# Kernel optimization log

Measured on AMD Instinct MI355X. Metric: run time of the kernel, lower is better.

## Reference

```python
import jax, jax.numpy as jnp
import numpy as np

P = 2          # inverse-distance power (init arg p)
EPS = 1e-6     # clamp floor on dis**p
B, N, D, VDIM = 4096, 8192, 512, 512


def setup_inputs() -> dict:
    key = jax.random.key(0)
    kb, kk, kv = jax.random.split(key, 3)
    b = jax.random.normal(kb, (B, D), dtype=jnp.float32)
    K = jax.random.normal(kk, (N, D), dtype=jnp.float32)   # stacked sample keys
    V = jax.random.normal(kv, (N, VDIM), dtype=jnp.float32)  # stacked sample values
    return {"b": b, "K": K, "V": V}


def reference(b, K, V):
    # Pairwise Euclidean distances via the expansion ||b-k||^2 = ||b||^2 + ||k||^2 - 2 b.k
    # (avoids materializing the [B, N, D] difference tensor).
    b_sq = jnp.sum(b * b, axis=1, keepdims=True)          # [B, 1]
    k_sq = jnp.sum(K * K, axis=1)[None, :]                # [1, N]
    d2 = b_sq + k_sq - 2.0 * (b @ K.T)                    # [B, N]
    dist = jnp.sqrt(jnp.maximum(d2, 0.0))                 # torch.norm(k - b, dim=1)
    w = 1.0 / jnp.maximum(dist ** P, EPS)                 # 1 / clamp(dis^p, 1e-6)
    sum_w = jnp.sum(w, axis=1, keepdims=True)             # [B, 1]
    sum_v = w @ V                                         # sum_n w[b,n] * V[n,:]
    return sum_v / sum_w
```

## Files before the change

kernel.cpp:

```cpp
#include <hip/hip_runtime.h>
#include <stdint.h>

typedef __attribute__((ext_vector_type(2))) float  f32x2;
typedef __attribute__((ext_vector_type(4))) float  f32x4;
typedef __attribute__((ext_vector_type(2))) __bf16 bf16x2;
typedef __attribute__((ext_vector_type(8))) __bf16 bf16x8;

#define N_B    4096
#define N_K    8192
#define DDIM   512
#define VD     512
#define SPLITK 4

#define GLL(g, l) __builtin_amdgcn_global_load_lds(                      \
    (const __attribute__((address_space(1))) void*)(g),                  \
    (__attribute__((address_space(3))) void*)(l), 16, 0, 0)

__global__ void prep_rows(const float* __restrict__ src, __bf16* __restrict__ dst,
                          float* __restrict__ sq)
{
  const int row = blockIdx.x;
  const int tid = threadIdx.x;
  f32x2 v = ((const f32x2*)(src + (size_t)row * DDIM))[tid];
  float ss = v[0] * v[0] + v[1] * v[1];
  bf16x2 o; o[0] = (__bf16)v[0]; o[1] = (__bf16)v[1];
  ((bf16x2*)(dst + (size_t)row * DDIM))[tid] = o;
  #pragma unroll
  for (int m = 1; m < 64; m <<= 1) ss += __shfl_xor(ss, m);
  __shared__ float red[4];
  if ((tid & 63) == 0) red[tid >> 6] = ss;
  __syncthreads();
  if (tid == 0) sq[row] = red[0] + red[1] + red[2] + red[3];
}

__global__ void prep_vT(const float* __restrict__ V, __bf16* __restrict__ VT)
{
  __shared__ __bf16 t[64][72];
  const int n0 = blockIdx.x * 64;
  const int d0 = blockIdx.y * 64;
  const int tid = threadIdx.x;
  const int lr = tid >> 4, lc = tid & 15;
  #pragma unroll
  for (int p = 0; p < 4; p++) {
    const int r = p * 16 + lr;
    f32x4 v = *(const f32x4*)(V + (size_t)(n0 + r) * VD + d0 + lc * 4);
    t[r][lc * 4 + 0] = (__bf16)v[0];
    t[r][lc * 4 + 1] = (__bf16)v[1];
    t[r][lc * 4 + 2] = (__bf16)v[2];
    t[r][lc * 4 + 3] = (__bf16)v[3];
  }
  __syncthreads();
  const int od = tid >> 6, oc = tid & 63;
  #pragma unroll
  for (int p = 0; p < 16; p++) {
    const int d = p * 4 + od;
    VT[(size_t)(d0 + d) * N_K + n0 + oc] = t[oc][d];
  }
}

template<int MODE>
__global__ void __launch_bounds__(256, 2)
gemm_bt(const __bf16* __restrict__ Amat, const __bf16* __restrict__ Bmat,
        const int ldaE, const int ldbE, const int kPerSplit,
        const float* __restrict__ bsq, const float* __restrict__ ksq,
        __bf16* __restrict__ Wout, float* __restrict__ sumw,
        float* __restrict__ Pout)
{
  __shared__ __bf16 Asm[128 * 64];
  __shared__ __bf16 Bsm[128 * 64];

  const int tid  = threadIdx.x;
  const int wid  = tid >> 6;
  const int lane = tid & 63;
  const int wm = wid >> 1, wn = wid & 1;
  const int r15 = lane & 15, hi = lane >> 4;

  const int m0 = blockIdx.y * 128;
  const int n0 = blockIdx.x * 128;
  const long kBegin = (long)blockIdx.z * kPerSplit;

  const int srow   = lane >> 3;
  const int schunk = (lane & 7) ^ srow;

  const __bf16* aSrc = Amat + (size_t)(m0 + wid * 32 + srow) * ldaE + kBegin + schunk * 8;
  const __bf16* bSrc = Bmat + (size_t)(n0 + wid * 32 + srow) * ldbE + kBegin + schunk * 8;
  __bf16* aDst = &Asm[wid * 32 * 64];
  __bf16* bDst = &Bsm[wid * 32 * 64];

  const f32x4 fzero = {0.f, 0.f, 0.f, 0.f};
  f32x4 acc[4][4];
  #pragma unroll
  for (int i = 0; i < 4; i++)
    #pragma unroll
    for (int j = 0; j < 4; j++) acc[i][j] = fzero;

  for (int k0 = 0; k0 < kPerSplit; k0 += 64) {
    __syncthreads();
    #pragma unroll
    for (int i = 0; i < 4; i++) {
      GLL(aSrc + (size_t)i * 8 * ldaE + k0, aDst + i * 8 * 64);
      GLL(bSrc + (size_t)i * 8 * ldbE + k0, bDst + i * 8 * 64);
    }
    __syncthreads();
    #pragma unroll
    for (int kk = 0; kk < 2; kk++) {
      bf16x8 af[4], bfr[4];
      #pragma unroll
      for (int mf = 0; mf < 4; mf++) {
        const int cs = ((kk << 2) + hi) ^ (r15 & 7);
        af[mf] = *(const bf16x8*)((const char*)Asm +
                   (wm * 64 + mf * 16 + r15) * 128 + cs * 16);
      }
      #pragma unroll
      for (int nf = 0; nf < 4; nf++) {
        const int cs = ((kk << 2) + hi) ^ (r15 & 7);
        bfr[nf] = *(const bf16x8*)((const char*)Bsm +
                    (wn * 64 + nf * 16 + r15) * 128 + cs * 16);
      }
      #pragma unroll
      for (int mf = 0; mf < 4; mf++)
        #pragma unroll
        for (int nf = 0; nf < 4; nf++)
          acc[mf][nf] = __builtin_amdgcn_mfma_f32_16x16x32_bf16(
              af[mf], bfr[nf], acc[mf][nf], 0, 0, 0);
    }
  }

  if constexpr (MODE == 0) {
    float kq[4];
    #pragma unroll
    for (int nf = 0; nf < 4; nf++) kq[nf] = ksq[n0 + wn * 64 + nf * 16 + r15];
    #pragma unroll
    for (int mf = 0; mf < 4; mf++) {
      const int rowb = m0 + wm * 64 + mf * 16 + hi * 4;
      const f32x4 bq = *(const f32x4*)(bsq + rowb);
      float rsum[4] = {0.f, 0.f, 0.f, 0.f};
      #pragma unroll
      for (int nf = 0; nf < 4; nf++) {
        const int col = n0 + wn * 64 + nf * 16 + r15;
        #pragma unroll
        for (int r = 0; r < 4; r++) {
          const float d2 = bq[r] + kq[nf] - 2.0f * acc[mf][nf][r];
          const float w  = 1.0f / fmaxf(d2, 1e-6f);
          rsum[r] += w;
          Wout[(size_t)(rowb + r) * N_K + col] = (__bf16)w;
        }
      }
      #pragma unroll
      for (int r = 0; r < 4; r++) {
        float tsum = rsum[r];
        tsum += __shfl_xor(tsum, 1);
        tsum += __shfl_xor(tsum, 2);
        tsum += __shfl_xor(tsum, 4);
        tsum += __shfl_xor(tsum, 8);
        if (r15 == 0) atomicAdd(&sumw[rowb + r], tsum);
      }
    }
  } else {
    float* op = Pout + (size_t)blockIdx.z * N_B * VD;
    #pragma unroll
    for (int mf = 0; mf < 4; mf++) {
      const int rowb = m0 + wm * 64 + mf * 16 + hi * 4;
      #pragma unroll
      for (int nf = 0; nf < 4; nf++) {
        const int col = n0 + wn * 64 + nf * 16 + r15;
        #pragma unroll
        for (int r = 0; r < 4; r++)
          op[(size_t)(rowb + r) * VD + col] = acc[mf][nf][r];
      }
    }
  }
}

__global__ void reduce_norm(const float* __restrict__ part, const float* __restrict__ sumw,
                            float* __restrict__ out)
{
  const int idx = blockIdx.x * 256 + threadIdx.x;
  const size_t stride = (size_t)N_B * VD / 4;
  const f32x4* p = (const f32x4*)part;
  f32x4 s = p[idx] + p[idx + stride] + p[idx + 2 * stride] + p[idx + 3 * stride];
  const float inv = 1.0f / sumw[idx >> 7];
  ((f32x4*)out)[idx] = s * inv;
}

extern "C" void kernel_launch(void* const* d_in, const int* in_sizes, int n_in,
                              void* d_out, int out_size, void* d_ws, size_t ws_size,
                              hipStream_t stream)
{
  const float* b = (const float*)d_in[0];
  const float* K = (const float*)d_in[1];
  const float* V = (const float*)d_in[2];
  float* out = (float*)d_out;
  (void)in_sizes; (void)n_in; (void)out_size; (void)ws_size;

  char* ws = (char*)d_ws;
  size_t off = 0;
  auto alloc = [&](size_t bytes) -> void* {
    void* p = ws + off;
    off += (bytes + 255) & ~(size_t)255;
    return p;
  };
  __bf16* b_bf  = (__bf16*)alloc((size_t)N_B * DDIM * 2);
  __bf16* K_bf  = (__bf16*)alloc((size_t)N_K * DDIM * 2);
  __bf16* V_T   = (__bf16*)alloc((size_t)VD * N_K * 2);
  float*  b_sq  = (float*)alloc((size_t)N_B * 4);
  float*  k_sq  = (float*)alloc((size_t)N_K * 4);
  float*  sum_w = (float*)alloc((size_t)N_B * 4);
  __bf16* w_bf  = (__bf16*)alloc((size_t)N_B * N_K * 2);
  float*  part  = (float*)alloc((size_t)SPLITK * N_B * VD * 4);

  hipMemsetAsync(sum_w, 0, N_B * 4, stream);
  prep_rows<<<N_B, 256, 0, stream>>>(b, b_bf, b_sq);
  prep_rows<<<N_K, 256, 0, stream>>>(K, K_bf, k_sq);
  prep_vT<<<dim3(N_K / 64, VD / 64), 256, 0, stream>>>(V, V_T);
  gemm_bt<0><<<dim3(N_K / 128, N_B / 128, 1), 256, 0, stream>>>(
      b_bf, K_bf, DDIM, DDIM, DDIM, b_sq, k_sq, w_bf, sum_w, nullptr);
  gemm_bt<1><<<dim3(VD / 128, N_B / 128, SPLITK), 256, 0, stream>>>(
      w_bf, V_T, N_K, N_K, N_K / SPLITK, nullptr, nullptr, nullptr, nullptr, part);
  reduce_norm<<<(N_B * VD / 4) / 256, 256, 0, stream>>>(part, sum_w, out);
}
```

Before: 213.2 us.

## Widen GEMM tiles to 128x256, fuse prep kernels, atomically accumulate split-K output

Merges the three prep kernels into one launch. Widens the GEMM block tile to 128x256, so each warp computes 64x128 with 32 accumulators, which raises operand reuse and register pressure. The distance-weight sums become deterministic per-block partials reduced by a separate kernel instead of atomics. The second GEMM doubles split-K to 8 and atomically adds into the zeroed output, replacing the partial buffer and its reduction pass. It adds a memset of the output, heavy atomic traffic and possible occupancy loss from the larger accumulator set.

```diff
diff --git a/kernel.cpp b/kernel.cpp
--- a/kernel.cpp
+++ b/kernel.cpp
@@ -10,51 +10,57 @@
 #define N_K    8192
 #define DDIM   512
 #define VD     512
-#define SPLITK 4
+#define SPLITK 8
 
 #define GLL(g, l) __builtin_amdgcn_global_load_lds(                      \
     (const __attribute__((address_space(1))) void*)(g),                  \
     (__attribute__((address_space(3))) void*)(l), 16, 0, 0)
 
-__global__ void prep_rows(const float* __restrict__ src, __bf16* __restrict__ dst,
-                          float* __restrict__ sq)
-{
-  const int row = blockIdx.x;
+__global__ void prep_all(const float* __restrict__ b, const float* __restrict__ K,
+                         const float* __restrict__ V,
+                         __bf16* __restrict__ b_bf, __bf16* __restrict__ K_bf,
+                         __bf16* __restrict__ VT,
+                         float* __restrict__ b_sq, float* __restrict__ k_sq)
+{
   const int tid = threadIdx.x;
-  f32x2 v = ((const f32x2*)(src + (size_t)row * DDIM))[tid];
-  float ss = v[0] * v[0] + v[1] * v[1];
-  bf16x2 o; o[0] = (__bf16)v[0]; o[1] = (__bf16)v[1];
-  ((bf16x2*)(dst + (size_t)row * DDIM))[tid] = o;
-  #pragma unroll
-  for (int m = 1; m < 64; m <<= 1) ss += __shfl_xor(ss, m);
-  __shared__ float red[4];
-  if ((tid & 63) == 0) red[tid >> 6] = ss;
-  __syncthreads();
-  if (tid == 0) sq[row] = red[0] + red[1] + red[2] + red[3];
-}
-
-__global__ void prep_vT(const float* __restrict__ V, __bf16* __restrict__ VT)
-{
-  __shared__ __bf16 t[64][72];
-  const int n0 = blockIdx.x * 64;
-  const int d0 = blockIdx.y * 64;
-  const int tid = threadIdx.x;
-  const int lr = tid >> 4, lc = tid & 15;
-  #pragma unroll
-  for (int p = 0; p < 4; p++) {
-    const int r = p * 16 + lr;
-    f32x4 v = *(const f32x4*)(V + (size_t)(n0 + r) * VD + d0 + lc * 4);
-    t[r][lc * 4 + 0] = (__bf16)v[0];
-    t[r][lc * 4 + 1] = (__bf16)v[1];
-    t[r][lc * 4 + 2] = (__bf16)v[2];
-    t[r][lc * 4 + 3] = (__bf16)v[3];
-  }
-  __syncthreads();
-  const int od = tid >> 6, oc = tid & 63;
-  #pragma unroll
-  for (int p = 0; p < 16; p++) {
-    const int d = p * 4 + od;
-    VT[(size_t)(d0 + d) * N_K + n0 + oc] = t[oc][d];
+  int bid = blockIdx.x;
+  if (bid < N_B + N_K) {
+    int row = bid;
+    const float* src; __bf16* dst; float* sq;
+    if (row < N_B) { src = b; dst = b_bf; sq = b_sq; }
+    else { row -= N_B; src = K; dst = K_bf; sq = k_sq; }
+    f32x2 v = ((const f32x2*)(src + (size_t)row * DDIM))[tid];
+    float ss = v[0] * v[0] + v[1] * v[1];
+    bf16x2 o; o[0] = (__bf16)v[0]; o[1] = (__bf16)v[1];
+    ((bf16x2*)(dst + (size_t)row * DDIM))[tid] = o;
+    #pragma unroll
+    for (int m = 1; m < 64; m <<= 1) ss += __shfl_xor(ss, m);
+    __shared__ float red[4];
+    if ((tid & 63) == 0) red[tid >> 6] = ss;
+    __syncthreads();
+    if (tid == 0) sq[row] = red[0] + red[1] + red[2] + red[3];
+  } else {
+    bid -= (N_B + N_K);
+    __shared__ __bf16 t[64][72];
+    const int n0 = (bid & 127) * 64;
+    const int d0 = (bid >> 7) * 64;
+    const int lr = tid >> 4, lc = tid & 15;
+    #pragma unroll
+    for (int p = 0; p < 4; p++) {
+      const int r = p * 16 + lr;
+      f32x4 v = *(const f32x4*)(V + (size_t)(n0 + r) * VD + d0 + lc * 4);
+      t[r][lc * 4 + 0] = (__bf16)v[0];
+      t[r][lc * 4 + 1] = (__bf16)v[1];
+      t[r][lc * 4 + 2] = (__bf16)v[2];
+      t[r][lc * 4 + 3] = (__bf16)v[3];
+    }
+    __syncthreads();
+    const int od = tid >> 6, oc = tid & 63;
+    #pragma unroll
+    for (int p = 0; p < 16; p++) {
+      const int d = p * 4 + od;
+      VT[(size_t)(d0 + d) * N_K + n0 + oc] = t[oc][d];
+    }
   }
 }
 
@@ -63,11 +69,11 @@
 gemm_bt(const __bf16* __restrict__ Amat, const __bf16* __restrict__ Bmat,
         const int ldaE, const int ldbE, const int kPerSplit,
         const float* __restrict__ bsq, const float* __restrict__ ksq,
-        __bf16* __restrict__ Wout, float* __restrict__ sumw,
+        __bf16* __restrict__ Wout, float* __restrict__ swPart,
         float* __restrict__ Pout)
 {
   __shared__ __bf16 Asm[128 * 64];
-  __shared__ __bf16 Bsm[128 * 64];
+  __shared__ __bf16 Bsm[256 * 64];
 
   const int tid  = threadIdx.x;
   const int wid  = tid >> 6;
@@ -76,68 +82,67 @@
   const int r15 = lane & 15, hi = lane >> 4;
 
   const int m0 = blockIdx.y * 128;
-  const int n0 = blockIdx.x * 128;
+  const int n0 = blockIdx.x * 256;
   const long kBegin = (long)blockIdx.z * kPerSplit;
 
   const int srow   = lane >> 3;
   const int schunk = (lane & 7) ^ srow;
 
   const __bf16* aSrc = Amat + (size_t)(m0 + wid * 32 + srow) * ldaE + kBegin + schunk * 8;
-  const __bf16* bSrc = Bmat + (size_t)(n0 + wid * 32 + srow) * ldbE + kBegin + schunk * 8;
+  const __bf16* bSrc = Bmat + (size_t)(n0 + wid * 64 + srow) * ldbE + kBegin + schunk * 8;
   __bf16* aDst = &Asm[wid * 32 * 64];
-  __bf16* bDst = &Bsm[wid * 32 * 64];
+  __bf16* bDst = &Bsm[wid * 64 * 64];
 
   const f32x4 fzero = {0.f, 0.f, 0.f, 0.f};
-  f32x4 acc[4][4];
+  f32x4 acc[4][8];
   #pragma unroll
   for (int i = 0; i < 4; i++)
     #pragma unroll
-    for (int j = 0; j < 4; j++) acc[i][j] = fzero;
+    for (int j = 0; j < 8; j++) acc[i][j] = fzero;
 
   for (int k0 = 0; k0 < kPerSplit; k0 += 64) {
     __syncthreads();
     #pragma unroll
-    for (int i = 0; i < 4; i++) {
+    for (int i = 0; i < 4; i++)
       GLL(aSrc + (size_t)i * 8 * ldaE + k0, aDst + i * 8 * 64);
+    #pragma unroll
+    for (int i = 0; i < 8; i++)
       GLL(bSrc + (size_t)i * 8 * ldbE + k0, bDst + i * 8 * 64);
-    }
+    asm volatile("s_waitcnt vmcnt(0)" ::: "memory");
     __syncthreads();
     #pragma unroll
     for (int kk = 0; kk < 2; kk++) {
-      bf16x8 af[4], bfr[4];
-      #pragma unroll
-      for (int mf = 0; mf < 4; mf++) {
-        const int cs = ((kk << 2) + hi) ^ (r15 & 7);
+      const int cs = ((kk << 2) + hi) ^ (r15 & 7);
+      bf16x8 af[4], bfr[8];
+      #pragma unroll
+      for (int mf = 0; mf < 4; mf++)
         af[mf] = *(const bf16x8*)((const char*)Asm +
                    (wm * 64 + mf * 16 + r15) * 128 + cs * 16);
-      }
-      #pragma unroll
-      for (int nf = 0; nf < 4; nf++) {
-        const int cs = ((kk << 2) + hi) ^ (r15 & 7);
+      #pragma unroll
+      for (int nf = 0; nf < 8; nf++)
         bfr[nf] = *(const bf16x8*)((const char*)Bsm +
-                    (wn * 64 + nf * 16 + r15) * 128 + cs * 16);
-      }
+                    (wn * 128 + nf * 16 + r15) * 128 + cs * 16);
       #pragma unroll
       for (int mf = 0; mf < 4; mf++)
         #pragma unroll
-        for (int nf = 0; nf < 4; nf++)
+        for (int nf = 0; nf < 8; nf++)
           acc[mf][nf] = __builtin_amdgcn_mfma_f32_16x16x32_bf16(
               af[mf], bfr[nf], acc[mf][nf], 0, 0, 0);
     }
   }
 
   if constexpr (MODE == 0) {
-    float kq[4];
-    #pragma unroll
-    for (int nf = 0; nf < 4; nf++) kq[nf] = ksq[n0 + wn * 64 + nf * 16 + r15];
+    float kq[8];
+    #pragma unroll
+    for (int nf = 0; nf < 8; nf++) kq[nf] = ksq[n0 + wn * 128 + nf * 16 + r15];
     #pragma unroll
     for (int mf = 0; mf < 4; mf++) {
       const int rowb = m0 + wm * 64 + mf * 16 + hi * 4;
       const f32x4 bq = *(const f32x4*)(bsq + rowb);
       float rsum[4] = {0.f, 0.f, 0.f, 0.f};
       #pragma unroll
-      for (int nf = 0; nf < 4; nf++) {
-        const int col = n0 + wn * 64 + nf * 16 + r15;
+      for (int nf = 0; nf < 8; nf++) {
+        const int col = n0 + wn * 128 + nf * 16 + r15;
         #pragma unroll
         for (int r = 0; r < 4; r++) {
           const float d2 = bq[r] + kq[nf] - 2.0f * acc[mf][nf][r];
@@ -153,34 +158,40 @@
         tsum += __shfl_xor(tsum, 2);
         tsum += __shfl_xor(tsum, 4);
         tsum += __shfl_xor(tsum, 8);
-        if (r15 == 0) atomicAdd(&sumw[rowb + r], tsum);
+        if (r15 == 0)
+          swPart[(size_t)(rowb + r) * 64 + blockIdx.x * 2 + wn] = tsum;
       }
     }
   } else {
-    float* op = Pout + (size_t)blockIdx.z * N_B * VD;
     #pragma unroll
     for (int mf = 0; mf < 4; mf++) {
       const int rowb = m0 + wm * 64 + mf * 16 + hi * 4;
       #pragma unroll
-      for (int nf = 0; nf < 4; nf++) {
-        const int col = n0 + wn * 64 + nf * 16 + r15;
+      for (int nf = 0; nf < 8; nf++) {
+        const int col = n0 + wn * 128 + nf * 16 + r15;
         #pragma unroll
         for (int r = 0; r < 4; r++)
-          op[(size_t)(rowb + r) * VD + col] = acc[mf][nf][r];
+          atomicAdd(&Pout[(size_t)(rowb + r) * VD + col], acc[mf][nf][r]);
       }
     }
   }
 }
 
-__global__ void reduce_norm(const float* __restrict__ part, const float* __restrict__ sumw,
-                            float* __restrict__ out)
+__global__ void sumw_reduce(const float* __restrict__ swPart, float* __restrict__ invSw)
+{
+  const int row  = blockIdx.x * 4 + (threadIdx.x >> 6);
+  const int lane = threadIdx.x & 63;
+  float s = swPart[(size_t)row * 64 + lane];
+  #pragma unroll
+  for (int m = 1; m < 64; m <<= 1) s += __shfl_xor(s, m);
+  if (lane == 0) invSw[row] = 1.0f / s;
+}
+
+__global__ void normalize(float* __restrict__ out, const float* __restrict__ invSw)
 {
   const int idx = blockIdx.x * 256 + threadIdx.x;
-  const size_t stride = (size_t)N_B * VD / 4;
-  const f32x4* p = (const f32x4*)part;
-  f32x4 s = p[idx] + p[idx + stride] + p[idx + 2 * stride] + p[idx + 3 * stride];
-  const float inv = 1.0f / sumw[idx >> 7];
-  ((f32x4*)out)[idx] = s * inv;
+  f32x4 v = ((f32x4*)out)[idx];
+  ((f32x4*)out)[idx] = v * invSw[idx >> 7];
 }
 
 extern "C" void kernel_launch(void* const* d_in, const int* in_sizes, int n_in,
@@ -191,7 +202,7 @@
   const float* K = (const float*)d_in[1];
   const float* V = (const float*)d_in[2];
   float* out = (float*)d_out;
-  (void)in_sizes; (void)n_in; (void)out_size; (void)ws_size;
+  (void)in_sizes; (void)n_in; (void)ws_size;
 
   char* ws = (char*)d_ws;
   size_t off = 0;
@@ -205,17 +216,17 @@
   __bf16* V_T   = (__bf16*)alloc((size_t)VD * N_K * 2);
   float*  b_sq  = (float*)alloc((size_t)N_B * 4);
   float*  k_sq  = (float*)alloc((size_t)N_K * 4);
-  float*  sum_w = (float*)alloc((size_t)N_B * 4);
+  float*  swp   = (float*)alloc((size_t)N_B * 64 * 4);
+  float*  invSw = (float*)alloc((size_t)N_B * 4);
   __bf16* w_bf  = (__bf16*)alloc((size_t)N_B * N_K * 2);
-  float*  part  = (float*)alloc((size_t)SPLITK * N_B * VD * 4);
-
-  hipMemsetAsync(sum_w, 0, N_B * 4, stream);
-  prep_rows<<<N_B, 256, 0, stream>>>(b, b_bf, b_sq);
-  prep_rows<<<N_K, 256, 0, stream>>>(K, K_bf, k_sq);
-  prep_vT<<<dim3(N_K / 64, VD / 64), 256, 0, stream>>>(V, V_T);
-  gemm_bt<0><<<dim3(N_K / 128, N_B / 128, 1), 256, 0, stream>>>(
-      b_bf, K_bf, DDIM, DDIM, DDIM, b_sq, k_sq, w_bf, sum_w, nullptr);
-  gemm_bt<1><<<dim3(VD / 128, N_B / 128, SPLITK), 256, 0, stream>>>(
-      w_bf, V_T, N_K, N_K, N_K / SPLITK, nullptr, nullptr, nullptr, nullptr, part);
-  reduce_norm<<<(N_B * VD / 4) / 256, 256, 0, stream>>>(part, sum_w, out);
-}
+
+  hipMemsetAsync(out, 0, (size_t)out_size * 4, stream);
+  prep_all<<<(N_B + N_K) + (N_K / 64) * (VD / 64), 256, 0, stream>>>(
+      b, K, V, b_bf, K_bf, V_T, b_sq, k_sq);
+  gemm_bt<0><<<dim3(N_K / 256, N_B / 128, 1), 256, 0, stream>>>(
+      b_bf, K_bf, DDIM, DDIM, DDIM, b_sq, k_sq, w_bf, swp, nullptr);
+  sumw_reduce<<<N_B / 4, 256, 0, stream>>>(swp, invSw);
+  gemm_bt<1><<<dim3(VD / 256, N_B / 128, SPLITK), 256, 0, stream>>>(
+      w_bf, V_T, N_K, N_K, N_K / SPLITK, nullptr, nullptr, nullptr, nullptr, out);
+  normalize<<<(N_B * VD / 4) / 256, 256, 0, stream>>>(out, invSw);
+}
```

After: 221.3 us. 3.8% more time.
